# Kernel tuning notes

Hardware: AMD Instinct MI355X
Metric: run time of the kernel (lower is better)

## Reference

```python
import jax, jax.numpy as jnp
import numpy as np

N, IN, OUT, H = 8192, 128, 64, 4
NEG_SLOPE = 0.2   # GATConv leaky-relu slope
EPS = 1e-5        # BatchNorm1d eps
MASK_VAL = -1e9   # masked_fill value for non-edges (finite for grad safety)


def setup_inputs() -> dict:
    key = jax.random.key(0)
    ks = jax.random.split(key, 5)
    x = jax.random.normal(ks[0], (N, IN), jnp.float32)
    adj = jax.random.randint(ks[1], (N, N), 0, 2, jnp.int32)  # dense 0/1 adjacency
    W = jax.random.normal(ks[2], (H, IN, OUT), jnp.float32) * (1.0 / np.sqrt(IN))
    a_i = jax.random.normal(ks[3], (H, OUT), jnp.float32) * (1.0 / np.sqrt(OUT))
    a_j = jax.random.normal(ks[4], (H, OUT), jnp.float32) * (1.0 / np.sqrt(OUT))
    gamma = jnp.ones((H * OUT,), jnp.float32)   # BN weight
    beta = jnp.zeros((H * OUT,), jnp.float32)   # BN bias
    return {"x": x, "adj": adj, "W": W, "a_i": a_i, "a_j": a_j,
            "gamma": gamma, "beta": beta}


def reference(x, adj, W, a_i, a_j, gamma, beta):
    # --- GATConv (dense adjacency, multi-head, concat) ---
    h = jnp.einsum('ni,hio->hno', x, W)              # [H, N, OUT]
    ei = jnp.einsum('hno,ho->hn', h, a_i)            # [H, N] source scores
    ej = jnp.einsum('hno,ho->hn', h, a_j)            # [H, N] target scores
    coe = ei[:, :, None] + ej[:, None, :]            # [H, N, N]
    coe = jnp.where(coe >= 0, coe, NEG_SLOPE * coe)  # leaky_relu
    coe = jnp.where(adj[None, :, :] == 0, MASK_VAL, coe)
    att = jax.nn.softmax(coe, axis=-1)               # segment softmax over neighbors
    out = jnp.einsum('hnm,hmo->hno', att, h)         # weighted aggregation
    out = jnp.transpose(out, (1, 0, 2)).reshape(N, H * OUT)  # concat heads
    # --- BatchNorm1d (training-mode batch stats over nodes) ---
    mean = jnp.mean(out, axis=0)
    var = jnp.var(out, axis=0)
    out = (out - mean) * jax.lax.rsqrt(var + EPS) * gamma + beta
    # --- ReLU ---
    return jax.nn.relu(out)
```

## Files before the change

### kernel.cpp

```cpp
#include <hip/hip_runtime.h>
#include <hip/hip_bf16.h>

#define NN   8192
#define IND  128
#define OUTD 64
#define NH   4
#define NEG_SLOPE 0.2f
#define BN_EPS 1e-5f

typedef __attribute__((ext_vector_type(8))) short bf16x8;
typedef __attribute__((ext_vector_type(4))) float f32x4;
typedef __attribute__((ext_vector_type(4))) int   i32x4;

static __device__ __forceinline__ float bf2f(short s) {
    union { unsigned u; float f; } v; v.u = ((unsigned)(unsigned short)s) << 16; return v.f;
}
static __device__ __forceinline__ short f2bf(float f) {
    union { float f; unsigned u; } v; v.f = f;
    return (short)((v.u + 0x8000u) >> 16);
}

__global__ __launch_bounds__(256) void k0_repackW(const float* __restrict__ W,
                                                  short* __restrict__ WB) {
    int tid = blockIdx.x * 256 + threadIdx.x;
    int o = tid & 63, i = (tid >> 6) & 127, h = tid >> 13;
    WB[((h * 16 + (i >> 3)) * 64 + o) * 8 + (i & 7)] = f2bf(W[(h * 128 + i) * 64 + o]);
}

__global__ __launch_bounds__(256) void k1_feat(const float* __restrict__ x,
                                               const short* __restrict__ WB,
                                               const float* __restrict__ a_i,
                                               const float* __restrict__ a_j,
                                               short* __restrict__ hB,
                                               float* __restrict__ t_ei,  float* __restrict__ t_E1i,
                                               float* __restrict__ t_E2i, float* __restrict__ t_nj,
                                               float* __restrict__ t_E1j, float* __restrict__ t_E2j) {
    int w = threadIdx.x >> 6;
    int l = threadIdx.x & 63;
    int quad = l >> 4, lx = l & 15;
    int rb = blockIdx.x;

    f32x4 acc[4] = {};
#pragma unroll
    for (int ks = 0; ks < 4; ++ks) {
        const float* xp = x + (rb * 16 + lx) * IND + ks * 32 + quad * 8;
        f32x4 xa = *(const f32x4*)xp;
        f32x4 xb = *(const f32x4*)(xp + 4);
        bf16x8 af;
#pragma unroll
        for (int j = 0; j < 4; ++j) { af[j] = f2bf(xa[j]); af[4 + j] = f2bf(xb[j]); }
#pragma unroll
        for (int ot = 0; ot < 4; ++ot) {
            bf16x8 bf = *(const bf16x8*)(WB + ((w * 16 + ks * 4 + quad) * 64 + ot * 16 + lx) * 8);
            acc[ot] = __builtin_amdgcn_mfma_f32_16x16x32_bf16(af, bf, acc[ot], 0, 0, 0);
        }
    }
    float aiv[4], ajv[4];
#pragma unroll
    for (int ot = 0; ot < 4; ++ot) {
        aiv[ot] = a_i[w * 64 + ot * 16 + lx];
        ajv[ot] = a_j[w * 64 + ot * 16 + lx];
    }
#pragma unroll
    for (int reg = 0; reg < 4; ++reg) {
        int row = rb * 16 + quad * 4 + reg;
        float ei = 0.f, ej = 0.f;
#pragma unroll
        for (int ot = 0; ot < 4; ++ot) {
            float hv = acc[ot][reg];
            ei += hv * aiv[ot];
            ej += hv * ajv[ot];
        }
#pragma unroll
        for (int m = 1; m <= 8; m <<= 1) {
            ei += __shfl_xor(ei, m, 64);
            ej += __shfl_xor(ej, m, 64);
        }
        if (lx == reg) {
            t_ei [w * NN + row] = ei;
            t_E1i[w * NN + row] = expf(ei);
            t_E2i[w * NN + row] = expf(NEG_SLOPE * ei);
            t_nj [w * NN + row] = -ej;
            t_E1j[w * NN + row] = expf(ej);
            t_E2j[w * NN + row] = expf(NEG_SLOPE * ej);
        }
#pragma unroll
        for (int ot = 0; ot < 4; ++ot) {
            int o = ot * 16 + lx;
            hB[((w * 1024 + (row >> 3)) * 64 + o) * 8 + (row & 7)] = f2bf(acc[ot][reg]);
        }
    }
}

__global__ __launch_bounds__(256) void k2_attn(const int* __restrict__ adj,
                                               const short* __restrict__ hB,
                                               const float* __restrict__ t_ei,
                                               const float* __restrict__ t_E1i,
                                               const float* __restrict__ t_E2i,
                                               const float* __restrict__ t_nj,
                                               const float* __restrict__ t_E1j,
                                               const float* __restrict__ t_E2j,
                                               float* __restrict__ num,
                                               float* __restrict__ Lsum) {
    int w = threadIdx.x >> 6;
    int l = threadIdx.x & 63;
    int quad = l >> 4, lx = l & 15;
    int rb = blockIdx.x >> 2, ks = blockIdx.x & 3;
    int rowbase = rb * 64;
    int tb = w * NN;

    float eiv[4], E1i[4], E2i[4];
#pragma unroll
    for (int r = 0; r < 4; ++r) {
        int i = rowbase + r * 16 + lx;
        eiv[r] = t_ei[tb + i];
        E1i[r] = t_E1i[tb + i];
        E2i[r] = t_E2i[tb + i];
    }

    f32x4 acc[4][4] = {};
    float Lacc[4] = {0.f, 0.f, 0.f, 0.f};
    int k0 = ks * 2048;

    i32x4 pa0[4], pa1[4];
    f32x4 pnj0, pnj1, pe10, pe11, pe20, pe21;
    {
        int kb = k0 + quad * 8;
        pnj0 = *(const f32x4*)(t_nj  + tb + kb);
        pnj1 = *(const f32x4*)(t_nj  + tb + kb + 4);
        pe10 = *(const f32x4*)(t_E1j + tb + kb);
        pe11 = *(const f32x4*)(t_E1j + tb + kb + 4);
        pe20 = *(const f32x4*)(t_E2j + tb + kb);
        pe21 = *(const f32x4*)(t_E2j + tb + kb + 4);
#pragma unroll
        for (int r = 0; r < 4; ++r) {
            const int* ap = adj + (size_t)(rowbase + r * 16 + lx) * NN + kb;
            pa0[r] = *(const i32x4*)ap;
            pa1[r] = *(const i32x4*)(ap + 4);
        }
    }

#pragma unroll 1
    for (int kt = 0; kt < 64; ++kt) {
        f32x4 nj0 = pnj0, nj1 = pnj1;
        f32x4 e1j0 = pe10, e1j1 = pe11;
        f32x4 e2j0 = pe20, e2j1 = pe21;
        i32x4 a0c[4], a1c[4];
#pragma unroll
        for (int r = 0; r < 4; ++r) { a0c[r] = pa0[r]; a1c[r] = pa1[r]; }

        int ktn = (kt + 1) & 63;
        int kbn = k0 + ktn * 32 + quad * 8;
        pnj0 = *(const f32x4*)(t_nj  + tb + kbn);
        pnj1 = *(const f32x4*)(t_nj  + tb + kbn + 4);
        pe10 = *(const f32x4*)(t_E1j + tb + kbn);
        pe11 = *(const f32x4*)(t_E1j + tb + kbn + 4);
        pe20 = *(const f32x4*)(t_E2j + tb + kbn);
        pe21 = *(const f32x4*)(t_E2j + tb + kbn + 4);
#pragma unroll
        for (int r = 0; r < 4; ++r) {
            const int* ap = adj + (size_t)(rowbase + r * 16 + lx) * NN + kbn;
            pa0[r] = *(const i32x4*)ap;
            pa1[r] = *(const i32x4*)(ap + 4);
        }

        int kb = k0 + kt * 32 + quad * 8;
        bf16x8 bfrag[4];
#pragma unroll
        for (int ot = 0; ot < 4; ++ot)
            bfrag[ot] = *(const bf16x8*)(hB + ((w * 1024 + (kb >> 3)) * 64 + ot * 16 + lx) * 8);

        bf16x8 afr[4];
#pragma unroll
        for (int r = 0; r < 4; ++r) {
            union { i32x4 i; bf16x8 b; } af;
            float lsum = 0.f;
#pragma unroll
            for (int jj = 0; jj < 4; ++jj) {
                int j0 = 2 * jj, j1 = 2 * jj + 1;
                int   av0 = (j0 < 4) ? a0c[r][j0] : a1c[r][j0 - 4];
                int   av1 = (j1 < 4) ? a0c[r][j1] : a1c[r][j1 - 4];
                float njA = (j0 < 4) ? nj0[j0] : nj1[j0 - 4];
                float njB = (j1 < 4) ? nj0[j1] : nj1[j1 - 4];
                float e1A = (j0 < 4) ? e1j0[j0] : e1j1[j0 - 4];
                float e1B = (j1 < 4) ? e1j0[j1] : e1j1[j1 - 4];
                float e2A = (j0 < 4) ? e2j0[j0] : e2j1[j0 - 4];
                float e2B = (j1 < 4) ? e2j0[j1] : e2j1[j1 - 4];
                bool  cA  = eiv[r] >= njA;
                bool  cB  = eiv[r] >= njB;
                float p0  = (cA ? E1i[r] : E2i[r]) * (cA ? e1A : e2A);
                float p1  = (cB ? E1i[r] : E2i[r]) * (cB ? e1B : e2B);
                p0 = av0 ? p0 : 0.0f;
                p1 = av1 ? p1 : 0.0f;
                lsum += p0 + p1;
                unsigned u0 = __float_as_uint(p0) + 0x8000u;
                unsigned u1 = __float_as_uint(p1) + 0x8000u;
                af.i[jj] = (int)__builtin_amdgcn_perm(u1, u0, 0x07060302);
            }
            Lacc[r] += lsum;
            afr[r] = af.b;
        }
#pragma unroll
        for (int r = 0; r < 4; ++r)
#pragma unroll
            for (int ot = 0; ot < 4; ++ot)
                acc[r][ot] = __builtin_amdgcn_mfma_f32_16x16x32_bf16(afr[r], bfrag[ot], acc[r][ot], 0, 0, 0);
    }

#pragma unroll
    for (int r = 0; r < 4; ++r) {
        float L = Lacc[r];
        L += __shfl_xor(L, 16, 64);
        L += __shfl_xor(L, 32, 64);
        if (l < 16)
            atomicAdd(&Lsum[w * NN + rowbase + r * 16 + lx], L);
    }
#pragma unroll
    for (int r = 0; r < 4; ++r)
#pragma unroll
        for (int ot = 0; ot < 4; ++ot)
#pragma unroll
            for (int reg = 0; reg < 4; ++reg) {
                int row = rowbase + r * 16 + quad * 4 + reg;
                atomicAdd(&num[row * 256 + w * 64 + ot * 16 + lx], acc[r][ot][reg]);
            }
}

__global__ __launch_bounds__(256) void k3_combine(float* __restrict__ num,
                                                  const float* __restrict__ Lsum,
                                                  float* __restrict__ stats) {
    int c = threadIdx.x;
    int h = c >> 6;
    float s = 0.f, s2 = 0.f;
    for (int rr = 0; rr < 32; ++rr) {
        int row = blockIdx.x * 32 + rr;
        float L = Lsum[h * NN + row];
        float val = num[row * 256 + c] / L;
        num[row * 256 + c] = val;
        s += val; s2 += val * val;
    }
    atomicAdd(&stats[c], s);
    atomicAdd(&stats[c + 256], s2);
}

__global__ __launch_bounds__(256) void k4_bnfinal(const float* __restrict__ stats,
                                                  const float* __restrict__ gamma,
                                                  const float* __restrict__ beta,
                                                  float* __restrict__ bnp) {
    int c = threadIdx.x;
    float mean = stats[c] * (1.0f / NN);
    float var  = stats[c + 256] * (1.0f / NN) - mean * mean;
    float sc = gamma[c] * rsqrtf(var + BN_EPS);
    bnp[c] = sc;
    bnp[c + 256] = beta[c] - mean * sc;
}

__global__ __launch_bounds__(256) void k5_apply(const float* __restrict__ preout,
                                                const float* __restrict__ bnp,
                                                float* __restrict__ out) {
    int g = blockIdx.x * 256 + threadIdx.x;
    f32x4 v = *(const f32x4*)(preout + (size_t)g * 4);
    int cb = (g * 4) & 255;
    f32x4 r;
#pragma unroll
    for (int j = 0; j < 4; ++j)
        r[j] = fmaxf(v[j] * bnp[cb + j] + bnp[256 + cb + j], 0.0f);
    *(f32x4*)(out + (size_t)g * 4) = r;
}

extern "C" void kernel_launch(void* const* d_in, const int* in_sizes, int n_in,
                              void* d_out, int out_size, void* d_ws, size_t ws_size,
                              hipStream_t stream) {
    (void)in_sizes; (void)n_in; (void)out_size; (void)ws_size;
    const float* x     = (const float*)d_in[0];
    const int*   adj   = (const int*)d_in[1];
    const float* W     = (const float*)d_in[2];
    const float* a_i   = (const float*)d_in[3];
    const float* a_j   = (const float*)d_in[4];
    const float* gamma = (const float*)d_in[5];
    const float* beta  = (const float*)d_in[6];
    float* out = (float*)d_out;

    char* ws = (char*)d_ws;
    short* WB    = (short*)(ws + 0);
    short* hB    = (short*)(ws + 65536);
    float* t_ei  = (float*)(ws + 4259840);
    float* t_E1i = t_ei + 32768;
    float* t_E2i = t_ei + 2 * 32768;
    float* t_nj  = t_ei + 3 * 32768;
    float* t_E1j = t_ei + 4 * 32768;
    float* t_E2j = t_ei + 5 * 32768;
    float* num   = (float*)(ws + 5046272);
    float* Lsum  = (float*)(ws + 13434880);
    float* stats = (float*)(ws + 13565952);
    float* bnp   = (float*)(ws + 13568000);

    hipMemsetAsync(num, 0, 8388608 + 131072 + 2048, stream);

    k0_repackW<<<dim3(128), dim3(256), 0, stream>>>(W, WB);
    k1_feat   <<<dim3(512), dim3(256), 0, stream>>>(x, WB, a_i, a_j, hB,
                                                    t_ei, t_E1i, t_E2i, t_nj, t_E1j, t_E2j);
    k2_attn   <<<dim3(512), dim3(256), 0, stream>>>(adj, hB, t_ei, t_E1i, t_E2i,
                                                    t_nj, t_E1j, t_E2j, num, Lsum);
    k3_combine<<<dim3(256), dim3(256), 0, stream>>>(num, Lsum, stats);
    k4_bnfinal<<<dim3(1),   dim3(256), 0, stream>>>(stats, gamma, beta, bnp);
    k5_apply  <<<dim3(2048), dim3(256), 0, stream>>>(num, bnp, out);
}
```

Measured before the change: 492.3 us.

## Precompress adjacency into a bitmask and fuse memset and BN finalize

A new pre-pass streams the int32 adjacency once and packs it into a 1-bit-per-edge bitmask. The attention kernel then reads one byte of mask per 8 neighbours instead of two 16-byte int vectors, which cuts its load traffic and register pressure. The same pre-pass zeroes the accumulator buffers in place of the memset, and the BN parameter computation is folded into the apply kernel through shared memory. The cost is an extra full-bandwidth pass over the adjacency plus an 8 MB bitmask in the workspace.

```diff
diff --git a/kernel.cpp b/kernel.cpp
--- a/kernel.cpp
+++ b/kernel.cpp
@@ -12,12 +12,29 @@
 typedef __attribute__((ext_vector_type(4))) float f32x4;
 typedef __attribute__((ext_vector_type(4))) int   i32x4;
 
-static __device__ __forceinline__ float bf2f(short s) {
-    union { unsigned u; float f; } v; v.u = ((unsigned)(unsigned short)s) << 16; return v.f;
-}
 static __device__ __forceinline__ short f2bf(float f) {
     union { float f; unsigned u; } v; v.f = f;
     return (short)((v.u + 0x8000u) >> 16);
+}
+
+__global__ __launch_bounds__(256) void kP_mask(const int* __restrict__ adj,
+                                               unsigned int* __restrict__ bm,
+                                               float* __restrict__ zreg) {
+    int tid = blockIdx.x * 256 + threadIdx.x;
+    for (int z = tid; z < 532608; z += 524288)
+        ((f32x4*)zreg)[z] = (f32x4){0.f, 0.f, 0.f, 0.f};
+    for (int wd = tid; wd < NN * NN / 32; wd += 524288) {
+        const int* ap = adj + (size_t)wd * 32;
+        unsigned m = 0;
+#pragma unroll
+        for (int q = 0; q < 8; ++q) {
+            i32x4 a = *(const i32x4*)(ap + q * 4);
+#pragma unroll
+            for (int j = 0; j < 4; ++j)
+                m |= (a[j] ? 1u : 0u) << (q * 4 + j);
+        }
+        bm[wd] = m;
+    }
 }
 
 __global__ __launch_bounds__(256) void k0_repackW(const float* __restrict__ W,
@@ -92,7 +109,7 @@
     }
 }
 
-__global__ __launch_bounds__(256) void k2_attn(const int* __restrict__ adj,
+__global__ __launch_bounds__(256) void k2_attn(const unsigned char* __restrict__ bmb,
                                                const short* __restrict__ hB,
                                                const float* __restrict__ t_ei,
                                                const float* __restrict__ t_E1i,
@@ -110,19 +127,21 @@
     int tb = w * NN;
 
     float eiv[4], E1i[4], E2i[4];
+    int mbase[4];
 #pragma unroll
     for (int r = 0; r < 4; ++r) {
         int i = rowbase + r * 16 + lx;
         eiv[r] = t_ei[tb + i];
         E1i[r] = t_E1i[tb + i];
         E2i[r] = t_E2i[tb + i];
+        mbase[r] = i * 1024 + ks * 256 + quad;
     }
 
     f32x4 acc[4][4] = {};
     float Lacc[4] = {0.f, 0.f, 0.f, 0.f};
     int k0 = ks * 2048;
 
-    i32x4 pa0[4], pa1[4];
+    int pm[4];
     f32x4 pnj0, pnj1, pe10, pe11, pe20, pe21;
     {
         int kb = k0 + quad * 8;
@@ -133,11 +152,7 @@
         pe20 = *(const f32x4*)(t_E2j + tb + kb);
         pe21 = *(const f32x4*)(t_E2j + tb + kb + 4);
 #pragma unroll
-        for (int r = 0; r < 4; ++r) {
-            const int* ap = adj + (size_t)(rowbase + r * 16 + lx) * NN + kb;
-            pa0[r] = *(const i32x4*)ap;
-            pa1[r] = *(const i32x4*)(ap + 4);
-        }
+        for (int r = 0; r < 4; ++r) pm[r] = bmb[mbase[r]];
     }
 
 #pragma unroll 1
@@ -145,9 +160,9 @@
         f32x4 nj0 = pnj0, nj1 = pnj1;
         f32x4 e1j0 = pe10, e1j1 = pe11;
         f32x4 e2j0 = pe20, e2j1 = pe21;
-        i32x4 a0c[4], a1c[4];
-#pragma unroll
-        for (int r = 0; r < 4; ++r) { a0c[r] = pa0[r]; a1c[r] = pa1[r]; }
+        int mc[4];
+#pragma unroll
+        for (int r = 0; r < 4; ++r) mc[r] = pm[r];
 
         int ktn = (kt + 1) & 63;
         int kbn = k0 + ktn * 32 + quad * 8;
@@ -158,11 +173,7 @@
         pe20 = *(const f32x4*)(t_E2j + tb + kbn);
         pe21 = *(const f32x4*)(t_E2j + tb + kbn + 4);
 #pragma unroll
-        for (int r = 0; r < 4; ++r) {
-            const int* ap = adj + (size_t)(rowbase + r * 16 + lx) * NN + kbn;
-            pa0[r] = *(const i32x4*)ap;
-            pa1[r] = *(const i32x4*)(ap + 4);
-        }
+        for (int r = 0; r < 4; ++r) pm[r] = bmb[mbase[r] + ktn * 4];
 
         int kb = k0 + kt * 32 + quad * 8;
         bf16x8 bfrag[4];
@@ -178,8 +189,8 @@
 #pragma unroll
             for (int jj = 0; jj < 4; ++jj) {
                 int j0 = 2 * jj, j1 = 2 * jj + 1;
-                int   av0 = (j0 < 4) ? a0c[r][j0] : a1c[r][j0 - 4];
-                int   av1 = (j1 < 4) ? a0c[r][j1] : a1c[r][j1 - 4];
+                int   av0 = mc[r] & (1 << j0);
+                int   av1 = mc[r] & (1 << j1);
                 float njA = (j0 < 4) ? nj0[j0] : nj1[j0 - 4];
                 float njB = (j1 < 4) ? nj0[j1] : nj1[j1 - 4];
                 float e1A = (j0 < 4) ? e1j0[j0] : e1j1[j0 - 4];
@@ -243,28 +254,27 @@
     atomicAdd(&stats[c + 256], s2);
 }
 
-__global__ __launch_bounds__(256) void k4_bnfinal(const float* __restrict__ stats,
-                                                  const float* __restrict__ gamma,
-                                                  const float* __restrict__ beta,
-                                                  float* __restrict__ bnp) {
+__global__ __launch_bounds__(256) void k5_apply(const float* __restrict__ preout,
+                                                const float* __restrict__ stats,
+                                                const float* __restrict__ gamma,
+                                                const float* __restrict__ beta,
+                                                float* __restrict__ out) {
+    __shared__ float sbnp[512];
     int c = threadIdx.x;
     float mean = stats[c] * (1.0f / NN);
     float var  = stats[c + 256] * (1.0f / NN) - mean * mean;
     float sc = gamma[c] * rsqrtf(var + BN_EPS);
-    bnp[c] = sc;
-    bnp[c + 256] = beta[c] - mean * sc;
-}
-
-__global__ __launch_bounds__(256) void k5_apply(const float* __restrict__ preout,
-                                                const float* __restrict__ bnp,
-                                                float* __restrict__ out) {
+    sbnp[c] = sc;
+    sbnp[c + 256] = beta[c] - mean * sc;
+    __syncthreads();
+
     int g = blockIdx.x * 256 + threadIdx.x;
     f32x4 v = *(const f32x4*)(preout + (size_t)g * 4);
     int cb = (g * 4) & 255;
     f32x4 r;
 #pragma unroll
     for (int j = 0; j < 4; ++j)
-        r[j] = fmaxf(v[j] * bnp[cb + j] + bnp[256 + cb + j], 0.0f);
+        r[j] = fmaxf(v[j] * sbnp[cb + j] + sbnp[256 + cb + j], 0.0f);
     *(f32x4*)(out + (size_t)g * 4) = r;
 }
 
@@ -293,16 +303,15 @@
     float* num   = (float*)(ws + 5046272);
     float* Lsum  = (float*)(ws + 13434880);
     float* stats = (float*)(ws + 13565952);
-    float* bnp   = (float*)(ws + 13568000);
-
-    hipMemsetAsync(num, 0, 8388608 + 131072 + 2048, stream);
-
-    k0_repackW<<<dim3(128), dim3(256), 0, stream>>>(W, WB);
-    k1_feat   <<<dim3(512), dim3(256), 0, stream>>>(x, WB, a_i, a_j, hB,
-                                                    t_ei, t_E1i, t_E2i, t_nj, t_E1j, t_E2j);
-    k2_attn   <<<dim3(512), dim3(256), 0, stream>>>(adj, hB, t_ei, t_E1i, t_E2i,
-                                                    t_nj, t_E1j, t_E2j, num, Lsum);
-    k3_combine<<<dim3(256), dim3(256), 0, stream>>>(num, Lsum, stats);
-    k4_bnfinal<<<dim3(1),   dim3(256), 0, stream>>>(stats, gamma, beta, bnp);
-    k5_apply  <<<dim3(2048), dim3(256), 0, stream>>>(num, bnp, out);
-}
+    unsigned int* bm = (unsigned int*)(ws + 13568000);
+
+    kP_mask   <<<dim3(2048), dim3(256), 0, stream>>>(adj, bm, num);
+    k0_repackW<<<dim3(128),  dim3(256), 0, stream>>>(W, WB);
+    k1_feat   <<<dim3(512),  dim3(256), 0, stream>>>(x, WB, a_i, a_j, hB,
+                                                     t_ei, t_E1i, t_E2i, t_nj, t_E1j, t_E2j);
+    k2_attn   <<<dim3(512),  dim3(256), 0, stream>>>((const unsigned char*)bm, hB,
+                                                     t_ei, t_E1i, t_E2i, t_nj, t_E1j, t_E2j,
+                                                     num, Lsum);
+    k3_combine<<<dim3(256),  dim3(256), 0, stream>>>(num, Lsum, stats);
+    k5_apply  <<<dim3(2048), dim3(256), 0, stream>>>(num, stats, gamma, beta, out);
+}
```

Measured after the change: 522.1 us. 6.1% more time.
